# Kernel optimization log

Hardware: AMD Instinct MI355X
Metric: run time of the kernel (lower is better)

Reference implementation:

```python
import jax, jax.numpy as jnp
import numpy as np

B, I, D = 2048, 4096, 512          # batch of candidates, num rated items, item_dim
IE, UE = 512, 1024                 # item_emb, user_emb
D1, D2, D3 = 1024, 512, 256        # MLP dense widths


def setup_inputs() -> dict:
    key = jax.random.key(0)
    ks = jax.random.split(key, 16)
    s = 0.02  # weight init scale
    candidate_items = jax.random.normal(ks[0], (B, D), dtype=jnp.float32)
    rated_items = jax.random.normal(ks[1], (I, D), dtype=jnp.float32)
    ratings = jax.random.uniform(ks[2], (B, I), dtype=jnp.float32, minval=0.5, maxval=5.0)
    keep = jax.random.uniform(ks[3], (B, I)) < 0.05
    user_matrix = jnp.where(keep, ratings, 0.0)
    return dict(
        candidate_items=candidate_items,
        rated_items=rated_items,
        user_matrix=user_matrix,
        att_w=jax.random.normal(ks[4], (2 * D, 1), dtype=jnp.float32) * s,
        att_b=jnp.zeros((1,), jnp.float32),
        iw1=jax.random.normal(ks[5], (D, 2 * IE), dtype=jnp.float32) * s,
        ib1=jnp.zeros((2 * IE,), jnp.float32),
        iw2=jax.random.normal(ks[6], (2 * IE, IE), dtype=jnp.float32) * s,
        ib2=jnp.zeros((IE,), jnp.float32),
        uw1=jax.random.normal(ks[7], (D, 2 * UE), dtype=jnp.float32) * s,
        ub1=jnp.zeros((2 * UE,), jnp.float32),
        uw2=jax.random.normal(ks[8], (2 * UE, UE), dtype=jnp.float32) * s,
        ub2=jnp.zeros((UE,), jnp.float32),
        mw1=jax.random.normal(ks[9], (IE + UE, D1), dtype=jnp.float32) * s,
        mb1=jnp.zeros((D1,), jnp.float32),
        mw2=jax.random.normal(ks[10], (D1, D2), dtype=jnp.float32) * s,
        mb2=jnp.zeros((D2,), jnp.float32),
        mw3=jax.random.normal(ks[11], (D2, D3), dtype=jnp.float32) * s,
        mb3=jnp.zeros((D3,), jnp.float32),
        mw4=jax.random.normal(ks[12], (D3, 1), dtype=jnp.float32) * s,
        mb4=jnp.zeros((1,), jnp.float32),
    )


def reference(candidate_items, rated_items, user_matrix,
              att_w, att_b, iw1, ib1, iw2, ib2, uw1, ub1, uw2, ub2,
              mw1, mb1, mw2, mb2, mw3, mb3, mw4, mb4):
    d = candidate_items.shape[1]
    # AttentionNet(Linear(2D,1)) on cat(cand_repeat, rated_tile) decomposes exactly:
    # score[b,i] = cand[b] @ w_c + rated[i] @ w_r + b  (same math, no (B*I,2D) blowup)
    wc, wr = att_w[:d], att_w[d:]                      # (D,1), (D,1)
    scores = candidate_items @ wc + (rated_items @ wr).T + att_b  # (B, I)
    scores = jnp.where(user_matrix == 0.0, -jnp.inf, scores)
    att = jax.nn.softmax(scores, axis=1)
    att = jnp.nan_to_num(att, nan=0.0, posinf=0.0, neginf=0.0)  # rows with no ratings -> 0
    user_feat = (att * user_matrix) @ rated_items      # (B, D)
    # dual towers (dropout = identity in eval)
    item_emb = jax.nn.relu(jax.nn.relu(candidate_items @ iw1 + ib1) @ iw2 + ib2)
    user_emb = jax.nn.relu(jax.nn.relu(user_feat @ uw1 + ub1) @ uw2 + ub2)
    x = jnp.concatenate([item_emb, user_emb], axis=1)  # (B, IE+UE)
    x = jax.nn.relu(x @ mw1 + mb1)
    x = jax.nn.relu(x @ mw2 + mb2)
    x = jax.nn.relu(x @ mw3 + mb3)
    return x @ mw4 + mb4                               # (B, 1)
```

## Files before the change

kernel.cpp:

```cpp
#include <hip/hip_runtime.h>
#include <cstddef>

constexpr int Bn = 2048;
constexpr int In = 4096;
constexpr int Dn = 512;

typedef _Float16 f16;
typedef _Float16 f16x8 __attribute__((ext_vector_type(8)));
typedef float    f32x4 __attribute__((ext_vector_type(4)));

__global__ __launch_bounds__(256) void k_rs(const float* __restrict__ rated,
                                            const float* __restrict__ att_w,
                                            float* __restrict__ rs) {
  const int wid  = threadIdx.x >> 6;
  const int lane = threadIdx.x & 63;
  const int i = blockIdx.x * 4 + wid;
  const float* row = rated + (size_t)i * Dn;
  const float* wr  = att_w + Dn;
  float s = 0.f;
  #pragma unroll
  for (int d = 0; d < Dn / 64; ++d)
    s = fmaf(row[lane + d * 64], wr[lane + d * 64], s);
  #pragma unroll
  for (int off = 32; off > 0; off >>= 1) s += __shfl_down(s, off);
  if (lane == 0) rs[i] = s;
}

__global__ __launch_bounds__(256) void k_att(const float* __restrict__ um,
                                             const float* __restrict__ rs,
                                             f16* __restrict__ att) {
  __shared__ float t[In];
  __shared__ float red[4];
  const int tid = threadIdx.x;
  const int b = blockIdx.x;
  const float* umrow = um + (size_t)b * In;

  float ua[16];
  float lmax = -INFINITY;
  #pragma unroll
  for (int it = 0; it < 4; ++it) {
    const int i = (it * 256 + tid) * 4;
    const float4 v = *reinterpret_cast<const float4*>(umrow + i);
    ua[it * 4 + 0] = v.x; ua[it * 4 + 1] = v.y;
    ua[it * 4 + 2] = v.z; ua[it * 4 + 3] = v.w;
    #pragma unroll
    for (int j = 0; j < 4; ++j) {
      if (ua[it * 4 + j] != 0.f) {
        const float r = rs[i + j];
        t[i + j] = r;
        lmax = fmaxf(lmax, r);
      } else {
        t[i + j] = -INFINITY;
      }
    }
  }
  #pragma unroll
  for (int off = 32; off > 0; off >>= 1) lmax = fmaxf(lmax, __shfl_down(lmax, off));
  if ((tid & 63) == 0) red[tid >> 6] = lmax;
  __syncthreads();
  const float m = fmaxf(fmaxf(red[0], red[1]), fmaxf(red[2], red[3]));
  __syncthreads();

  float lsum = 0.f;
  #pragma unroll
  for (int it = 0; it < 4; ++it) {
    const int i = (it * 256 + tid) * 4;
    #pragma unroll
    for (int j = 0; j < 4; ++j) {
      float v = 0.f;
      if (ua[it * 4 + j] != 0.f) {
        const float e = __expf(t[i + j] - m);
        lsum += e;
        v = e * ua[it * 4 + j];
      }
      t[i + j] = v;
    }
  }
  #pragma unroll
  for (int off = 32; off > 0; off >>= 1) lsum += __shfl_down(lsum, off);
  if ((tid & 63) == 0) red[tid >> 6] = lsum;
  __syncthreads();
  const float S = red[0] + red[1] + red[2] + red[3];
  const float inv = (S > 0.f) ? 1.0f / S : 0.0f;

  f16* arow = att + (size_t)b * In;
  #pragma unroll
  for (int it = 0; it < 2; ++it) {
    const int i = (it * 256 + tid) * 8;
    f16x8 h;
    #pragma unroll
    for (int j = 0; j < 8; ++j) h[j] = (f16)(t[i + j] * inv);
    *reinterpret_cast<f16x8*>(arow + i) = h;
  }
}

__global__ __launch_bounds__(256) void k_transpose_f2h(const float* __restrict__ src,
                                                       f16* __restrict__ dst,
                                                       int K, int N) {
  __shared__ float tile[32][33];
  const int tx = threadIdx.x & 31;
  const int ty = threadIdx.x >> 5;
  const int n0 = blockIdx.x * 32;
  const int k0 = blockIdx.y * 32;
  #pragma unroll
  for (int i = 0; i < 4; ++i)
    tile[ty + i * 8][tx] = src[(size_t)(k0 + ty + i * 8) * N + n0 + tx];
  __syncthreads();
  #pragma unroll
  for (int i = 0; i < 4; ++i)
    dst[(size_t)(n0 + ty + i * 8) * K + k0 + tx] = (f16)tile[tx][ty + i * 8];
}

__global__ __launch_bounds__(256) void k_cast_f2h(const float* __restrict__ src,
                                                  f16* __restrict__ dst, int n) {
  const int i = (blockIdx.x * 256 + threadIdx.x) * 4;
  if (i < n) {
    const float4 v = *reinterpret_cast<const float4*>(src + i);
    f16 h0 = (f16)v.x, h1 = (f16)v.y, h2 = (f16)v.z, h3 = (f16)v.w;
    f16* p = dst + i;
    p[0] = h0; p[1] = h1; p[2] = h2; p[3] = h3;
  }
}

struct GemmDesc {
  const f16* A;
  const f16* Wt;
  const float* bias;
  f16* C;
  float* P;
  int N, K, Kc, ldc, nTilesN, relu;
};

__global__ __launch_bounds__(256) void k_mgemm(GemmDesc dA, GemmDesc dB, int bSplit) {
  const bool second = ((int)blockIdx.x >= bSplit);
  const GemmDesc d = second ? dB : dA;
  const int local = second ? (int)blockIdx.x - bSplit : (int)blockIdx.x;

  const int bm = (local & 31) * 64;
  const int rest = local >> 5;
  const int bn = (rest % d.nTilesN) * 64;
  const int ks = rest / d.nTilesN;
  const int kBeg = ks * d.Kc;

  __shared__ __align__(16) f16 As[64][72];
  __shared__ __align__(16) f16 Bs[64][72];

  const int tid  = threadIdx.x;
  const int lane = tid & 63;
  const int wave = tid >> 6;
  const int wrow = (wave >> 1) * 32;
  const int wcol = (wave & 1) * 32;
  const int lrow = lane & 15;
  const int koff = (lane >> 4) * 8;

  const int r = tid >> 2;
  const int c = (tid & 3) * 16;

  const f16* pa = d.A  + (size_t)(bm + r) * d.K + kBeg + c;
  const f16* pb = d.Wt + (size_t)(bn + r) * d.K + kBeg + c;

  f16x8 ra0, ra1, rb0, rb1;
  #define LOADG()                                                   \
    ra0 = *reinterpret_cast<const f16x8*>(pa + 0);                  \
    ra1 = *reinterpret_cast<const f16x8*>(pa + 8);                  \
    rb0 = *reinterpret_cast<const f16x8*>(pb + 0);                  \
    rb1 = *reinterpret_cast<const f16x8*>(pb + 8);

  f32x4 acc[2][2] = {};

  LOADG();
  for (int k0 = 0; k0 < d.Kc; k0 += 64) {
    *reinterpret_cast<f16x8*>(&As[r][c + 0]) = ra0;
    *reinterpret_cast<f16x8*>(&As[r][c + 8]) = ra1;
    *reinterpret_cast<f16x8*>(&Bs[r][c + 0]) = rb0;
    *reinterpret_cast<f16x8*>(&Bs[r][c + 8]) = rb1;
    __syncthreads();

    if (k0 + 64 < d.Kc) {
      pa += 64; pb += 64;
      LOADG();
    }

    #pragma unroll
    for (int kss = 0; kss < 2; ++kss) {
      const int kk = kss * 32 + koff;
      const f16x8 a0 = *reinterpret_cast<const f16x8*>(&As[wrow +  0 + lrow][kk]);
      const f16x8 a1 = *reinterpret_cast<const f16x8*>(&As[wrow + 16 + lrow][kk]);
      const f16x8 b0 = *reinterpret_cast<const f16x8*>(&Bs[wcol +  0 + lrow][kk]);
      const f16x8 b1 = *reinterpret_cast<const f16x8*>(&Bs[wcol + 16 + lrow][kk]);

      acc[0][0] = __builtin_amdgcn_mfma_f32_16x16x32_f16(a0, b0, acc[0][0], 0, 0, 0);
      acc[0][1] = __builtin_amdgcn_mfma_f32_16x16x32_f16(a0, b1, acc[0][1], 0, 0, 0);
      acc[1][0] = __builtin_amdgcn_mfma_f32_16x16x32_f16(a1, b0, acc[1][0], 0, 0, 0);
      acc[1][1] = __builtin_amdgcn_mfma_f32_16x16x32_f16(a1, b1, acc[1][1], 0, 0, 0);
    }
    __syncthreads();
  }
  #undef LOADG

  const int orow = (lane >> 4) * 4;
  if (d.P) {
    float* pp = d.P + (size_t)ks * ((size_t)2048 * d.N);
    #pragma unroll
    for (int mf = 0; mf < 2; ++mf)
      #pragma unroll
      for (int nf = 0; nf < 2; ++nf) {
        const int col = bn + wcol + nf * 16 + lrow;
        #pragma unroll
        for (int rr = 0; rr < 4; ++rr) {
          const int row = bm + wrow + mf * 16 + orow + rr;
          pp[(size_t)row * d.N + col] = acc[mf][nf][rr];
        }
      }
  } else {
    #pragma unroll
    for (int mf = 0; mf < 2; ++mf)
      #pragma unroll
      for (int nf = 0; nf < 2; ++nf) {
        const int col = bn + wcol + nf * 16 + lrow;
        const float bv = d.bias ? d.bias[col] : 0.f;
        #pragma unroll
        for (int rr = 0; rr < 4; ++rr) {
          const int row = bm + wrow + mf * 16 + orow + rr;
          float v = acc[mf][nf][rr] + bv;
          if (d.relu) v = fmaxf(v, 0.f);
          d.C[(size_t)row * d.ldc + col] = (f16)v;
        }
      }
  }
}

__global__ __launch_bounds__(256) void k_reduce(const float* __restrict__ P,
                                                int S, int MN, int N,
                                                const float* __restrict__ bias,
                                                int relu, f16* __restrict__ C,
                                                int ldc) {
  const int idx = (blockIdx.x * 256 + threadIdx.x) * 8;
  float v[8];
  {
    const float4 a0 = *reinterpret_cast<const float4*>(P + idx);
    const float4 a1 = *reinterpret_cast<const float4*>(P + idx + 4);
    v[0] = a0.x; v[1] = a0.y; v[2] = a0.z; v[3] = a0.w;
    v[4] = a1.x; v[5] = a1.y; v[6] = a1.z; v[7] = a1.w;
  }
  for (int s = 1; s < S; ++s) {
    const float* ps = P + (size_t)s * MN + idx;
    const float4 b0 = *reinterpret_cast<const float4*>(ps);
    const float4 b1 = *reinterpret_cast<const float4*>(ps + 4);
    v[0] += b0.x; v[1] += b0.y; v[2] += b0.z; v[3] += b0.w;
    v[4] += b1.x; v[5] += b1.y; v[6] += b1.z; v[7] += b1.w;
  }
  const int row = idx / N;
  const int col = idx % N;
  f16x8 h;
  #pragma unroll
  for (int j = 0; j < 8; ++j) {
    float x = v[j] + (bias ? bias[col + j] : 0.f);
    if (relu) x = fmaxf(x, 0.f);
    h[j] = (f16)x;
  }
  *reinterpret_cast<f16x8*>(C + (size_t)row * ldc + col) = h;
}

__global__ __launch_bounds__(256) void k_final(const f16* __restrict__ h3,
                                               const float* __restrict__ mw4,
                                               const float* __restrict__ mb4,
                                               float* __restrict__ out) {
  const int wid = threadIdx.x >> 6;
  const int lane = threadIdx.x & 63;
  const int row = blockIdx.x * 4 + wid;
  const f16* hr = h3 + (size_t)row * 256;
  float s = 0.f;
  #pragma unroll
  for (int d = 0; d < 4; ++d)
    s = fmaf((float)hr[lane + d * 64], mw4[lane + d * 64], s);
  #pragma unroll
  for (int off = 32; off > 0; off >>= 1) s += __shfl_down(s, off);
  if (lane == 0) out[row] = s + mb4[0];
}

extern "C" void kernel_launch(void* const* d_in, const int* in_sizes, int n_in,
                              void* d_out, int out_size, void* d_ws, size_t ws_size,
                              hipStream_t stream) {
  const float* cand  = (const float*)d_in[0];
  const float* rated = (const float*)d_in[1];
  const float* um    = (const float*)d_in[2];
  const float* att_w = (const float*)d_in[3];
  const float* iw1 = (const float*)d_in[5];
  const float* ib1 = (const float*)d_in[6];
  const float* iw2 = (const float*)d_in[7];
  const float* ib2 = (const float*)d_in[8];
  const float* uw1 = (const float*)d_in[9];
  const float* ub1 = (const float*)d_in[10];
  const float* uw2 = (const float*)d_in[11];
  const float* ub2 = (const float*)d_in[12];
  const float* mw1 = (const float*)d_in[13];
  const float* mb1 = (const float*)d_in[14];
  const float* mw2 = (const float*)d_in[15];
  const float* mb2 = (const float*)d_in[16];
  const float* mw3 = (const float*)d_in[17];
  const float* mb3 = (const float*)d_in[18];
  const float* mw4 = (const float*)d_in[19];
  const float* mb4 = (const float*)d_in[20];
  float* out = (float*)d_out;

  f16*   hws = (f16*)d_ws;
  float* rs  = (float*)d_ws;
  size_t off = 8192;
  auto take = [&](size_t n) { f16* p = hws + off; off += n; return p; };
  f16* t_iw1   = take(512 * 1024);
  f16* t_iw2   = take(1024 * 512);
  f16* t_uw1   = take(512 * 2048);
  f16* t_uw2   = take(2048 * 1024);
  f16* t_mw1   = take(1536 * 1024);
  f16* t_mw2   = take(1024 * 512);
  f16* t_mw3   = take(512 * 256);
  f16* t_rated = take(512 * 4096);
  f16* cand_h  = take(2048 * 512);
  f16* uf_h    = take(2048 * 512);
  f16* big     = take(2048 * 2048);
  f16* Xc      = take(2048 * 1536);
  f16* spare   = take(2048 * 512);
  f16* h_i1b   = take(2048 * 1024);
  float* Pbuf  = (float*)take(8 * 1024 * 1024);
  (void)spare;
  f16* att_d = big;
  f16* h_u1 = big;
  f16* h_m1 = big;
  f16* h_m2 = uf_h;
  f16* h_m3 = cand_h;

  dim3 blk(256);

  k_rs<<<dim3(In / 4), blk, 0, stream>>>(rated, att_w, rs);
  k_att<<<dim3(Bn), blk, 0, stream>>>(um, rs, att_d);

  k_transpose_f2h<<<dim3( 512/32, 4096/32), blk, 0, stream>>>(rated, t_rated, 4096, 512);
  k_transpose_f2h<<<dim3(1024/32,  512/32), blk, 0, stream>>>(iw1, t_iw1,  512, 1024);
  k_transpose_f2h<<<dim3( 512/32, 1024/32), blk, 0, stream>>>(iw2, t_iw2, 1024,  512);
  k_transpose_f2h<<<dim3(2048/32,  512/32), blk, 0, stream>>>(uw1, t_uw1,  512, 2048);
  k_transpose_f2h<<<dim3(1024/32, 2048/32), blk, 0, stream>>>(uw2, t_uw2, 2048, 1024);
  k_transpose_f2h<<<dim3(1024/32, 1536/32), blk, 0, stream>>>(mw1, t_mw1, 1536, 1024);
  k_transpose_f2h<<<dim3( 512/32, 1024/32), blk, 0, stream>>>(mw2, t_mw2, 1024,  512);
  k_transpose_f2h<<<dim3( 256/32,  512/32), blk, 0, stream>>>(mw3, t_mw3,  512,  256);
  k_cast_f2h<<<dim3(Bn * Dn / 1024), blk, 0, stream>>>(cand, cand_h, Bn * Dn);

  GemmDesc dUF = { att_d, t_rated, nullptr, nullptr, Pbuf, 512, 4096, 1024, 512, 8, 0 };
  GemmDesc dI1 = { cand_h, t_iw1, ib1, h_i1b, nullptr, 1024, 512, 512, 1024, 16, 1 };
  GemmDesc dU1 = { uf_h, t_uw1, ub1, h_u1, nullptr, 2048, 512, 512, 2048, 32, 1 };
  GemmDesc dI2 = { h_i1b, t_iw2, ib2, Xc, nullptr, 512, 1024, 1024, 1536, 8, 1 };
  GemmDesc dU2 = { h_u1, t_uw2, nullptr, nullptr, Pbuf, 1024, 2048, 1024, 1536, 16, 1 };
  GemmDesc dM1 = { Xc, t_mw1, nullptr, nullptr, Pbuf, 1024, 1536, 768, 1024, 16, 1 };
  GemmDesc dM2 = { h_m1, t_mw2, nullptr, nullptr, Pbuf, 512, 1024, 256, 512, 8, 1 };
  GemmDesc dM3 = { h_m2, t_mw3, nullptr, nullptr, Pbuf, 256, 512, 128, 256, 4, 1 };

  k_mgemm<<<dim3(1536), blk, 0, stream>>>(dUF, dI1, 1024);
  k_reduce<<<dim3(512), blk, 0, stream>>>(Pbuf, 4, 2048 * 512, 512, nullptr, 0, uf_h, 512);

  k_mgemm<<<dim3(1280), blk, 0, stream>>>(dU1, dI2, 1024);

  k_mgemm<<<dim3(1024), blk, 0, stream>>>(dU2, dU2, 1024);
  k_reduce<<<dim3(1024), blk, 0, stream>>>(Pbuf, 2, 2048 * 1024, 1024, ub2, 1, Xc + 512, 1536);

  k_mgemm<<<dim3(1024), blk, 0, stream>>>(dM1, dM1, 1024);
  k_reduce<<<dim3(1024), blk, 0, stream>>>(Pbuf, 2, 2048 * 1024, 1024, mb1, 1, h_m1, 1024);

  k_mgemm<<<dim3(1024), blk, 0, stream>>>(dM2, dM2, 1024);
  k_reduce<<<dim3(512), blk, 0, stream>>>(Pbuf, 4, 2048 * 512, 512, mb2, 1, h_m2, 512);

  k_mgemm<<<dim3(512), blk, 0, stream>>>(dM3, dM3, 512);
  k_reduce<<<dim3(256), blk, 0, stream>>>(Pbuf, 4, 2048 * 256, 256, mb3, 1, h_m3, 256);

  k_final<<<dim3(Bn / 4), blk, 0, stream>>>(h_m3, mw4, mb4, out);
}
```

Before: 292.7 us.

## Use 128x128 GEMM tiles, batch prep kernels, fuse last MLP layers into tail kernel

Tiles grow from 64x64 to 128x128, with each wave computing a 4x4 block of MFMA fragments, so each shared-memory load feeds more MFMAs. The eight transposes and the cast are merged into one descriptor-driven prep kernel, and reductions can now serve two GEMMs in one launch. The mw3 GEMM plus the final dot product are replaced by a single scalar tail kernel. Larger tiles halve the block count, which risks underfilling the CUs on the smaller GEMMs, and the scalar tail avoids MFMA entirely.

```diff
diff --git a/kernel.cpp b/kernel.cpp
--- a/kernel.cpp
+++ b/kernel.cpp
@@ -94,32 +94,35 @@
   }
 }
 
-__global__ __launch_bounds__(256) void k_transpose_f2h(const float* __restrict__ src,
-                                                       f16* __restrict__ dst,
-                                                       int K, int N) {
+struct PrepDesc { const float* src; f16* dst; int K, N, nt, isCast; };
+struct PrepPack { PrepDesc d[9]; };
+
+__global__ __launch_bounds__(256) void k_prep(PrepPack pk) {
   __shared__ float tile[32][33];
-  const int tx = threadIdx.x & 31;
-  const int ty = threadIdx.x >> 5;
-  const int n0 = blockIdx.x * 32;
-  const int k0 = blockIdx.y * 32;
+  int local = blockIdx.x;
+  int q = 0;
+  while (local >= pk.d[q].nt) { local -= pk.d[q].nt; ++q; }
+  const PrepDesc dd = pk.d[q];
+  const int tid = threadIdx.x;
+
+  if (dd.isCast) {
+    const int i = (local * 256 + tid) * 4;
+    const float4 v = *reinterpret_cast<const float4*>(dd.src + i);
+    f16* p = dd.dst + i;
+    p[0] = (f16)v.x; p[1] = (f16)v.y; p[2] = (f16)v.z; p[3] = (f16)v.w;
+    return;
+  }
+  const int tx = tid & 31;
+  const int ty = tid >> 5;
+  const int n0 = (local % (dd.N / 32)) * 32;
+  const int k0 = (local / (dd.N / 32)) * 32;
   #pragma unroll
   for (int i = 0; i < 4; ++i)
-    tile[ty + i * 8][tx] = src[(size_t)(k0 + ty + i * 8) * N + n0 + tx];
+    tile[ty + i * 8][tx] = dd.src[(size_t)(k0 + ty + i * 8) * dd.N + n0 + tx];
   __syncthreads();
   #pragma unroll
   for (int i = 0; i < 4; ++i)
-    dst[(size_t)(n0 + ty + i * 8) * K + k0 + tx] = (f16)tile[tx][ty + i * 8];
-}
-
-__global__ __launch_bounds__(256) void k_cast_f2h(const float* __restrict__ src,
-                                                  f16* __restrict__ dst, int n) {
-  const int i = (blockIdx.x * 256 + threadIdx.x) * 4;
-  if (i < n) {
-    const float4 v = *reinterpret_cast<const float4*>(src + i);
-    f16 h0 = (f16)v.x, h1 = (f16)v.y, h2 = (f16)v.z, h3 = (f16)v.w;
-    f16* p = dst + i;
-    p[0] = h0; p[1] = h1; p[2] = h2; p[3] = h3;
-  }
+    dd.dst[(size_t)(n0 + ty + i * 8) * dd.K + k0 + tx] = (f16)tile[tx][ty + i * 8];
 }
 
 struct GemmDesc {
@@ -136,44 +139,52 @@
   const GemmDesc d = second ? dB : dA;
   const int local = second ? (int)blockIdx.x - bSplit : (int)blockIdx.x;
 
-  const int bm = (local & 31) * 64;
-  const int rest = local >> 5;
-  const int bn = (rest % d.nTilesN) * 64;
+  const int bm = (local & 15) * 128;
+  const int rest = local >> 4;
+  const int bn = (rest % d.nTilesN) * 128;
   const int ks = rest / d.nTilesN;
   const int kBeg = ks * d.Kc;
 
-  __shared__ __align__(16) f16 As[64][72];
-  __shared__ __align__(16) f16 Bs[64][72];
+  __shared__ __align__(16) f16 As[128][72];
+  __shared__ __align__(16) f16 Bs[128][72];
 
   const int tid  = threadIdx.x;
   const int lane = tid & 63;
   const int wave = tid >> 6;
-  const int wrow = (wave >> 1) * 32;
-  const int wcol = (wave & 1) * 32;
+  const int wrow = (wave >> 1) * 64;
+  const int wcol = (wave & 1) * 64;
   const int lrow = lane & 15;
   const int koff = (lane >> 4) * 8;
 
-  const int r = tid >> 2;
-  const int c = (tid & 3) * 16;
-
-  const f16* pa = d.A  + (size_t)(bm + r) * d.K + kBeg + c;
-  const f16* pb = d.Wt + (size_t)(bn + r) * d.K + kBeg + c;
-
-  f16x8 ra0, ra1, rb0, rb1;
+  const int ar = tid >> 1;
+  const int ac = (tid & 1) * 32;
+
+  const f16* pa = d.A  + (size_t)(bm + ar) * d.K + kBeg + ac;
+  const f16* pb = d.Wt + (size_t)(bn + ar) * d.K + kBeg + ac;
+
+  f16x8 ra0, ra1, ra2, ra3, rb0, rb1, rb2, rb3;
   #define LOADG()                                                   \
-    ra0 = *reinterpret_cast<const f16x8*>(pa + 0);                  \
-    ra1 = *reinterpret_cast<const f16x8*>(pa + 8);                  \
-    rb0 = *reinterpret_cast<const f16x8*>(pb + 0);                  \
-    rb1 = *reinterpret_cast<const f16x8*>(pb + 8);
-
-  f32x4 acc[2][2] = {};
+    ra0 = *reinterpret_cast<const f16x8*>(pa +  0);                 \
+    ra1 = *reinterpret_cast<const f16x8*>(pa +  8);                 \
+    ra2 = *reinterpret_cast<const f16x8*>(pa + 16);                 \
+    ra3 = *reinterpret_cast<const f16x8*>(pa + 24);                 \
+    rb0 = *reinterpret_cast<const f16x8*>(pb +  0);                 \
+    rb1 = *reinterpret_cast<const f16x8*>(pb +  8);                 \
+    rb2 = *reinterpret_cast<const f16x8*>(pb + 16);                 \
+    rb3 = *reinterpret_cast<const f16x8*>(pb + 24);
+
+  f32x4 acc[4][4] = {};
 
   LOADG();
   for (int k0 = 0; k0 < d.Kc; k0 += 64) {
-    *reinterpret_cast<f16x8*>(&As[r][c + 0]) = ra0;
-    *reinterpret_cast<f16x8*>(&As[r][c + 8]) = ra1;
-    *reinterpret_cast<f16x8*>(&Bs[r][c + 0]) = rb0;
-    *reinterpret_cast<f16x8*>(&Bs[r][c + 8]) = rb1;
+    *reinterpret_cast<f16x8*>(&As[ar][ac +  0]) = ra0;
+    *reinterpret_cast<f16x8*>(&As[ar][ac +  8]) = ra1;
+    *reinterpret_cast<f16x8*>(&As[ar][ac + 16]) = ra2;
+    *reinterpret_cast<f16x8*>(&As[ar][ac + 24]) = ra3;
+    *reinterpret_cast<f16x8*>(&Bs[ar][ac +  0]) = rb0;
+    *reinterpret_cast<f16x8*>(&Bs[ar][ac +  8]) = rb1;
+    *reinterpret_cast<f16x8*>(&Bs[ar][ac + 16]) = rb2;
+    *reinterpret_cast<f16x8*>(&Bs[ar][ac + 24]) = rb3;
     __syncthreads();
 
     if (k0 + 64 < d.Kc) {
@@ -184,15 +195,18 @@
     #pragma unroll
     for (int kss = 0; kss < 2; ++kss) {
       const int kk = kss * 32 + koff;
-      const f16x8 a0 = *reinterpret_cast<const f16x8*>(&As[wrow +  0 + lrow][kk]);
-      const f16x8 a1 = *reinterpret_cast<const f16x8*>(&As[wrow + 16 + lrow][kk]);
-      const f16x8 b0 = *reinterpret_cast<const f16x8*>(&Bs[wcol +  0 + lrow][kk]);
-      const f16x8 b1 = *reinterpret_cast<const f16x8*>(&Bs[wcol + 16 + lrow][kk]);
-
-      acc[0][0] = __builtin_amdgcn_mfma_f32_16x16x32_f16(a0, b0, acc[0][0], 0, 0, 0);
-      acc[0][1] = __builtin_amdgcn_mfma_f32_16x16x32_f16(a0, b1, acc[0][1], 0, 0, 0);
-      acc[1][0] = __builtin_amdgcn_mfma_f32_16x16x32_f16(a1, b0, acc[1][0], 0, 0, 0);
-      acc[1][1] = __builtin_amdgcn_mfma_f32_16x16x32_f16(a1, b1, acc[1][1], 0, 0, 0);
+      f16x8 a[4], b[4];
+      #pragma unroll
+      for (int m = 0; m < 4; ++m)
+        a[m] = *reinterpret_cast<const f16x8*>(&As[wrow + m * 16 + lrow][kk]);
+      #pragma unroll
+      for (int n = 0; n < 4; ++n)
+        b[n] = *reinterpret_cast<const f16x8*>(&Bs[wcol + n * 16 + lrow][kk]);
+      #pragma unroll
+      for (int m = 0; m < 4; ++m)
+        #pragma unroll
+        for (int n = 0; n < 4; ++n)
+          acc[m][n] = __builtin_amdgcn_mfma_f32_16x16x32_f16(a[m], b[n], acc[m][n], 0, 0, 0);
     }
     __syncthreads();
   }
@@ -202,9 +216,9 @@
   if (d.P) {
     float* pp = d.P + (size_t)ks * ((size_t)2048 * d.N);
     #pragma unroll
-    for (int mf = 0; mf < 2; ++mf)
-      #pragma unroll
-      for (int nf = 0; nf < 2; ++nf) {
+    for (int mf = 0; mf < 4; ++mf)
+      #pragma unroll
+      for (int nf = 0; nf < 4; ++nf) {
         const int col = bn + wcol + nf * 16 + lrow;
         #pragma unroll
         for (int rr = 0; rr < 4; ++rr) {
@@ -214,9 +228,9 @@
       }
   } else {
     #pragma unroll
-    for (int mf = 0; mf < 2; ++mf)
-      #pragma unroll
-      for (int nf = 0; nf < 2; ++nf) {
+    for (int mf = 0; mf < 4; ++mf)
+      #pragma unroll
+      for (int nf = 0; nf < 4; ++nf) {
         const int col = bn + wcol + nf * 16 + lrow;
         const float bv = d.bias ? d.bias[col] : 0.f;
         #pragma unroll
@@ -230,53 +244,84 @@
   }
 }
 
-__global__ __launch_bounds__(256) void k_reduce(const float* __restrict__ P,
-                                                int S, int MN, int N,
-                                                const float* __restrict__ bias,
-                                                int relu, f16* __restrict__ C,
-                                                int ldc) {
-  const int idx = (blockIdx.x * 256 + threadIdx.x) * 8;
+struct RedDesc {
+  const float* P; int S, MN, N;
+  const float* bias; int relu; f16* C; int ldc;
+};
+
+__global__ __launch_bounds__(256) void k_reduce2(RedDesc a, RedDesc b, int bSplit) {
+  const bool second = ((int)blockIdx.x >= bSplit);
+  const RedDesc d = second ? b : a;
+  const int local = second ? (int)blockIdx.x - bSplit : (int)blockIdx.x;
+  const int idx = (local * 256 + threadIdx.x) * 8;
+
   float v[8];
   {
-    const float4 a0 = *reinterpret_cast<const float4*>(P + idx);
-    const float4 a1 = *reinterpret_cast<const float4*>(P + idx + 4);
+    const float4 a0 = *reinterpret_cast<const float4*>(d.P + idx);
+    const float4 a1 = *reinterpret_cast<const float4*>(d.P + idx + 4);
     v[0] = a0.x; v[1] = a0.y; v[2] = a0.z; v[3] = a0.w;
     v[4] = a1.x; v[5] = a1.y; v[6] = a1.z; v[7] = a1.w;
   }
-  for (int s = 1; s < S; ++s) {
-    const float* ps = P + (size_t)s * MN + idx;
+  for (int s = 1; s < d.S; ++s) {
+    const float* ps = d.P + (size_t)s * d.MN + idx;
     const float4 b0 = *reinterpret_cast<const float4*>(ps);
     const float4 b1 = *reinterpret_cast<const float4*>(ps + 4);
     v[0] += b0.x; v[1] += b0.y; v[2] += b0.z; v[3] += b0.w;
     v[4] += b1.x; v[5] += b1.y; v[6] += b1.z; v[7] += b1.w;
   }
-  const int row = idx / N;
-  const int col = idx % N;
+  const int row = idx / d.N;
+  const int col = idx % d.N;
   f16x8 h;
   #pragma unroll
   for (int j = 0; j < 8; ++j) {
-    float x = v[j] + (bias ? bias[col + j] : 0.f);
-    if (relu) x = fmaxf(x, 0.f);
+    float x = v[j] + (d.bias ? d.bias[col + j] : 0.f);
+    if (d.relu) x = fmaxf(x, 0.f);
     h[j] = (f16)x;
   }
-  *reinterpret_cast<f16x8*>(C + (size_t)row * ldc + col) = h;
-}
-
-__global__ __launch_bounds__(256) void k_final(const f16* __restrict__ h3,
-                                               const float* __restrict__ mw4,
-                                               const float* __restrict__ mb4,
-                                               float* __restrict__ out) {
-  const int wid = threadIdx.x >> 6;
-  const int lane = threadIdx.x & 63;
-  const int row = blockIdx.x * 4 + wid;
-  const f16* hr = h3 + (size_t)row * 256;
-  float s = 0.f;
-  #pragma unroll
-  for (int d = 0; d < 4; ++d)
-    s = fmaf((float)hr[lane + d * 64], mw4[lane + d * 64], s);
-  #pragma unroll
-  for (int off = 32; off > 0; off >>= 1) s += __shfl_down(s, off);
-  if (lane == 0) out[row] = s + mb4[0];
+  *reinterpret_cast<f16x8*>(d.C + (size_t)row * d.ldc + col) = h;
+}
+
+__global__ __launch_bounds__(256) void k_tail(const f16* __restrict__ h2,
+                                              const f16* __restrict__ t_mw3,
+                                              const float* __restrict__ mb3,
+                                              const float* __restrict__ mw4,
+                                              const float* __restrict__ mb4,
+                                              float* __restrict__ out) {
+  __shared__ f16 rows[4][512];
+  __shared__ float red[4][4];
+  const int tid = threadIdx.x;
+  const int r0 = blockIdx.x * 4;
+
+  *reinterpret_cast<f16x8*>(&rows[tid >> 6][(tid & 63) * 8]) =
+      *reinterpret_cast<const f16x8*>(&h2[(size_t)(r0 + (tid >> 6)) * 512 + (tid & 63) * 8]);
+  __syncthreads();
+
+  const int j = tid;
+  float acc[4] = {};
+  for (int k = 0; k < 512; k += 8) {
+    const f16x8 w = *reinterpret_cast<const f16x8*>(&t_mw3[(size_t)j * 512 + k]);
+    #pragma unroll
+    for (int e = 0; e < 8; ++e) {
+      const float wf = (float)w[e];
+      #pragma unroll
+      for (int r = 0; r < 4; ++r)
+        acc[r] = fmaf(wf, (float)rows[r][k + e], acc[r]);
+    }
+  }
+  const float b3 = mb3[j];
+  const float m4 = mw4[j];
+  const int lane = tid & 63;
+  const int wid  = tid >> 6;
+  #pragma unroll
+  for (int r = 0; r < 4; ++r) {
+    float v = fmaxf(acc[r] + b3, 0.f) * m4;
+    #pragma unroll
+    for (int off = 32; off > 0; off >>= 1) v += __shfl_down(v, off);
+    if (lane == 0) red[r][wid] = v;
+  }
+  __syncthreads();
+  if (tid < 4)
+    out[r0 + tid] = red[tid][0] + red[tid][1] + red[tid][2] + red[tid][3] + mb4[0];
 }
 
 extern "C" void kernel_launch(void* const* d_in, const int* in_sizes, int n_in,
@@ -322,54 +367,62 @@
   f16* Xc      = take(2048 * 1536);
   f16* spare   = take(2048 * 512);
   f16* h_i1b   = take(2048 * 1024);
-  float* Pbuf  = (float*)take(8 * 1024 * 1024);
+  float* PA    = (float*)take(4 * 2048 * 512 * 2);
+  float* PB    = (float*)take(2 * 2048 * 1024 * 2);
   (void)spare;
   f16* att_d = big;
   f16* h_u1 = big;
   f16* h_m1 = big;
   f16* h_m2 = uf_h;
-  f16* h_m3 = cand_h;
 
   dim3 blk(256);
 
   k_rs<<<dim3(In / 4), blk, 0, stream>>>(rated, att_w, rs);
+  PrepPack pk = {{
+      { rated, t_rated, 4096,  512, (512/32)*(4096/32), 0 },
+      { iw1,   t_iw1,    512, 1024, (1024/32)*(512/32), 0 },
+      { iw2,   t_iw2,   1024,  512, (512/32)*(1024/32), 0 },
+      { uw1,   t_uw1,    512, 2048, (2048/32)*(512/32), 0 },
+      { uw2,   t_uw2,   2048, 1024, (1024/32)*(2048/32), 0 },
+      { mw1,   t_mw1,   1536, 1024, (1024/32)*(1536/32), 0 },
+      { mw2,   t_mw2,   1024,  512, (512/32)*(1024/32), 0 },
+      { mw3,   t_mw3,    512,  256, (256/32)*(512/32), 0 },
+      { cand,  cand_h,     0,    0, (Bn * Dn) / 1024, 1 },
+  }};
+  int prepGrid = 0;
+  for (int q = 0; q < 9; ++q) prepGrid += pk.d[q].nt;
+  k_prep<<<dim3(prepGrid), blk, 0, stream>>>(pk);
   k_att<<<dim3(Bn), blk, 0, stream>>>(um, rs, att_d);
 
-  k_transpose_f2h<<<dim3( 512/32, 4096/32), blk, 0, stream>>>(rated, t_rated, 4096, 512);
-  k_transpose_f2h<<<dim3(1024/32,  512/32), blk, 0, stream>>>(iw1, t_iw1,  512, 1024);
-  k_transpose_f2h<<<dim3( 512/32, 1024/32), blk, 0, stream>>>(iw2, t_iw2, 1024,  512);
-  k_transpose_f2h<<<dim3(2048/32,  512/32), blk, 0, stream>>>(uw1, t_uw1,  512, 2048);
-  k_transpose_f2h<<<dim3(1024/32, 2048/32), blk, 0, stream>>>(uw2, t_uw2, 2048, 1024);
-  k_transpose_f2h<<<dim3(1024/32, 1536/32), blk, 0, stream>>>(mw1, t_mw1, 1536, 1024);
-  k_transpose_f2h<<<dim3( 512/32, 1024/32), blk, 0, stream>>>(mw2, t_mw2, 1024,  512);
-  k_transpose_f2h<<<dim3( 256/32,  512/32), blk, 0, stream>>>(mw3, t_mw3,  512,  256);
-  k_cast_f2h<<<dim3(Bn * Dn / 1024), blk, 0, stream>>>(cand, cand_h, Bn * Dn);
-
-  GemmDesc dUF = { att_d, t_rated, nullptr, nullptr, Pbuf, 512, 4096, 1024, 512, 8, 0 };
-  GemmDesc dI1 = { cand_h, t_iw1, ib1, h_i1b, nullptr, 1024, 512, 512, 1024, 16, 1 };
-  GemmDesc dU1 = { uf_h, t_uw1, ub1, h_u1, nullptr, 2048, 512, 512, 2048, 32, 1 };
-  GemmDesc dI2 = { h_i1b, t_iw2, ib2, Xc, nullptr, 512, 1024, 1024, 1536, 8, 1 };
-  GemmDesc dU2 = { h_u1, t_uw2, nullptr, nullptr, Pbuf, 1024, 2048, 1024, 1536, 16, 1 };
-  GemmDesc dM1 = { Xc, t_mw1, nullptr, nullptr, Pbuf, 1024, 1536, 768, 1024, 16, 1 };
-  GemmDesc dM2 = { h_m1, t_mw2, nullptr, nullptr, Pbuf, 512, 1024, 256, 512, 8, 1 };
-  GemmDesc dM3 = { h_m2, t_mw3, nullptr, nullptr, Pbuf, 256, 512, 128, 256, 4, 1 };
-
-  k_mgemm<<<dim3(1536), blk, 0, stream>>>(dUF, dI1, 1024);
-  k_reduce<<<dim3(512), blk, 0, stream>>>(Pbuf, 4, 2048 * 512, 512, nullptr, 0, uf_h, 512);
-
-  k_mgemm<<<dim3(1280), blk, 0, stream>>>(dU1, dI2, 1024);
-
-  k_mgemm<<<dim3(1024), blk, 0, stream>>>(dU2, dU2, 1024);
-  k_reduce<<<dim3(1024), blk, 0, stream>>>(Pbuf, 2, 2048 * 1024, 1024, ub2, 1, Xc + 512, 1536);
-
-  k_mgemm<<<dim3(1024), blk, 0, stream>>>(dM1, dM1, 1024);
-  k_reduce<<<dim3(1024), blk, 0, stream>>>(Pbuf, 2, 2048 * 1024, 1024, mb1, 1, h_m1, 1024);
-
-  k_mgemm<<<dim3(1024), blk, 0, stream>>>(dM2, dM2, 1024);
-  k_reduce<<<dim3(512), blk, 0, stream>>>(Pbuf, 4, 2048 * 512, 512, mb2, 1, h_m2, 512);
-
-  k_mgemm<<<dim3(512), blk, 0, stream>>>(dM3, dM3, 512);
-  k_reduce<<<dim3(256), blk, 0, stream>>>(Pbuf, 4, 2048 * 256, 256, mb3, 1, h_m3, 256);
-
-  k_final<<<dim3(Bn / 4), blk, 0, stream>>>(h_m3, mw4, mb4, out);
-}
+  GemmDesc dUF = { att_d,  t_rated, nullptr, nullptr, PA, 512, 4096, 1024, 512, 4, 0 };
+  GemmDesc dI1 = { cand_h, t_iw1,   nullptr, nullptr, PB, 1024, 512, 256, 1024, 8, 1 };
+  GemmDesc dI2 = { h_i1b,  t_iw2,   nullptr, nullptr, PA, 512, 1024, 256, 1536, 4, 1 };
+  GemmDesc dU1 = { uf_h,   t_uw1,   ub1, h_u1, nullptr, 2048, 512, 512, 2048, 16, 1 };
+  GemmDesc dU2 = { h_u1,   t_uw2,   nullptr, nullptr, PA, 1024, 2048, 1024, 1536, 8, 1 };
+  GemmDesc dM1 = { Xc,     t_mw1,   nullptr, nullptr, PA, 1024, 1536, 768, 1024, 8, 1 };
+  GemmDesc dM2 = { h_m1,   t_mw2,   nullptr, nullptr, PA, 512, 1024, 256, 512, 4, 1 };
+
+  RedDesc rUF = { PA, 4, 2048 * 512,  512,  nullptr, 0, uf_h,  512 };
+  RedDesc rI1 = { PB, 2, 2048 * 1024, 1024, ib1, 1, h_i1b, 1024 };
+  RedDesc rI2 = { PA, 4, 2048 * 512,  512,  ib2, 1, Xc,       1536 };
+  RedDesc rU2 = { PA, 2, 2048 * 1024, 1024, ub2, 1, Xc + 512, 1536 };
+  RedDesc rM1 = { PA, 2, 2048 * 1024, 1024, mb1, 1, h_m1, 1024 };
+  RedDesc rM2 = { PA, 4, 2048 * 512,  512,  mb2, 1, h_m2, 512 };
+
+  k_mgemm<<<dim3(512), blk, 0, stream>>>(dUF, dI1, 256);
+  k_reduce2<<<dim3(512 + 1024), blk, 0, stream>>>(rUF, rI1, 512);
+
+  k_mgemm<<<dim3(512), blk, 0, stream>>>(dI2, dU1, 256);
+  k_reduce2<<<dim3(512), blk, 0, stream>>>(rI2, rI2, 512);
+
+  k_mgemm<<<dim3(256), blk, 0, stream>>>(dU2, dU2, 256);
+  k_reduce2<<<dim3(1024), blk, 0, stream>>>(rU2, rU2, 1024);
+
+  k_mgemm<<<dim3(256), blk, 0, stream>>>(dM1, dM1, 256);
+  k_reduce2<<<dim3(1024), blk, 0, stream>>>(rM1, rM1, 1024);
+
+  k_mgemm<<<dim3(256), blk, 0, stream>>>(dM2, dM2, 256);
+  k_reduce2<<<dim3(512), blk, 0, stream>>>(rM2, rM2, 512);
+
+  k_tail<<<dim3(Bn / 4), blk, 0, stream>>>(h_m2, t_mw3, mb3, mw4, mb4, out);
+}
```

Result: slower. 304.1 us (+3.9%).
